# Kernel tuning notes

Measured on AMD Instinct MI355X. Metric: run time of the kernel, lower is better.

The kernel has to match this reference:

```python
import jax, jax.numpy as jnp
import numpy as np

N, E, D_IN, D_OUT = 100000, 3200000, 128, 128


def setup_inputs() -> dict:
    key = jax.random.key(0)
    ks = jax.random.split(key, 6)
    return {
        "x": jax.random.normal(ks[0], (N, D_IN), dtype=jnp.float32),
        "row": jax.random.randint(ks[1], (E,), 0, N),
        "col": jax.random.randint(ks[2], (E,), 0, N),
        "W0": jax.random.normal(ks[3], (D_OUT, D_IN), dtype=jnp.float32) * (1.0 / np.sqrt(D_IN)),
        "b0": jnp.zeros((D_OUT,), jnp.float32),
        "W1": jax.random.normal(ks[4], (D_OUT, D_IN), dtype=jnp.float32) * (1.0 / np.sqrt(D_IN)),
        "b1": jnp.zeros((D_OUT,), jnp.float32),
        "att": jax.random.normal(ks[5], (2 * D_OUT,), dtype=jnp.float32) * 0.1,
        "scale0": jnp.ones((D_OUT,), jnp.float32),
        "offset0": jnp.zeros((D_OUT,), jnp.float32),
        "scale1": jnp.ones((D_OUT,), jnp.float32),
        "offset1": jnp.zeros((D_OUT,), jnp.float32),
    }


def _norm(f, scale, offset):
    # per-node normalization over feature dim (bias='norm' branch)
    m = jnp.mean(f, axis=1, keepdims=True)
    v = jnp.var(f, axis=1, keepdims=True) + 1e-9
    return (f - m) * scale * jax.lax.rsqrt(v) + offset


def reference(x, row, col, W0, b0, W1, b1, att, scale0, offset0, scale1, offset1):
    d = W0.shape[0]
    # order-0 (self) and order-1 (neighbor) feature transforms, act='relu'
    h0 = jax.nn.relu(x @ W0.T + b0)  # [N, d]
    h1 = jax.nn.relu(x @ W1.T + b1)  # [N, d]
    # unnormalized GAT attention (no softmax), LeakyReLU(0.2)
    a_self = jax.nn.leaky_relu(h0 @ att[:d], negative_slope=0.2)   # [N]
    a_neigh = jax.nn.leaky_relu(h1 @ att[d:], negative_slope=0.2)  # [N]
    e = a_self[row] + a_neigh[col]                                 # [E]
    # SpMM: out[i] = sum_{(i,j) in edges} e_ij * h1[j]
    agg = jax.ops.segment_sum(e[:, None] * h1[col], row, num_segments=h0.shape[0])
    # batch-norm style normalization per head, then mean-aggregate over orders
    out = _norm(h0, scale0, offset0) + _norm(agg, scale1, offset1)
    return out
```

## Files before the change

### kernel.cpp

```cpp
#include <hip/hip_runtime.h>
#include <hip/hip_bf16.h>

constexpr int D = 128;
constexpr int BUCKET_SHIFT = 6;
constexpr int BUCKET_CAP_LOG2 = 12;
constexpr int BUCKET_CAP = 1 << BUCKET_CAP_LOG2;
constexpr int SEG_SHIFT = 13;
constexpr int NSEG = 13;
constexpr int BINS_PER_BUCKET = 4 * NSEG * 16;
constexpr int BINS_PER_WAVE = NSEG * 16;
constexpr int ROWSTRIDE = 130;
typedef __hip_bfloat16 bf16;

__global__ __launch_bounds__(256) void k_gemm(
    const float* __restrict__ x,
    const float* __restrict__ W0, const float* __restrict__ b0,
    const float* __restrict__ W1, const float* __restrict__ b1,
    const float* __restrict__ att,
    float* __restrict__ h0, bf16* __restrict__ h1b,
    float* __restrict__ a_self, float* __restrict__ a_neigh, int N)
{
  constexpr int XS_STRIDE = 132;
  constexpr int WS_STRIDE = 68;
  __shared__ float xs_t[64 * XS_STRIDE];
  __shared__ float ws_t[64 * WS_STRIDE];

  const int t  = threadIdx.x;
  const int nb = blockIdx.x;
  const int fb = blockIdx.y;
  const int n0 = nb * 128;

  const float* __restrict__ W    = (fb < 2) ? W0 : W1;
  const float* __restrict__ bias = (fb < 2) ? b0 : b1;
  float* __restrict__ adest      = (fb < 2) ? a_self : a_neigh;
  const int frow0 = (fb & 1) * 64;

  const int tf = t & 15;
  const int tn = t >> 4;

  const int x_nq = t >> 1;
  const int x_kq = t & 1;
  const int w_f  = t >> 2;
  const int w_kq = t & 3;

  float acc[8][4];
#pragma unroll
  for (int i = 0; i < 8; ++i)
#pragma unroll
    for (int j = 0; j < 4; ++j) acc[i][j] = 0.0f;

  const bool x_ok = (n0 + x_nq) < N;
  const float* xrow = x + (size_t)(n0 + x_nq) * D;
  const float* wrow = W + (size_t)(frow0 + w_f) * D;

  for (int c = 0; c < 2; ++c) {
    const int k0 = c * 64;
    if (c) __syncthreads();

#pragma unroll
    for (int i = 0; i < 8; ++i) {
      const int k = x_kq * 32 + i * 4;
      float4 v = x_ok ? *reinterpret_cast<const float4*>(xrow + k0 + k)
                      : make_float4(0.f, 0.f, 0.f, 0.f);
      xs_t[(k + 0) * XS_STRIDE + x_nq] = v.x;
      xs_t[(k + 1) * XS_STRIDE + x_nq] = v.y;
      xs_t[(k + 2) * XS_STRIDE + x_nq] = v.z;
      xs_t[(k + 3) * XS_STRIDE + x_nq] = v.w;
    }
#pragma unroll
    for (int i = 0; i < 4; ++i) {
      const int k = w_kq * 4 + i * 16;
      float4 v = *reinterpret_cast<const float4*>(wrow + k0 + k);
      ws_t[(k + 0) * WS_STRIDE + w_f] = v.x;
      ws_t[(k + 1) * WS_STRIDE + w_f] = v.y;
      ws_t[(k + 2) * WS_STRIDE + w_f] = v.z;
      ws_t[(k + 3) * WS_STRIDE + w_f] = v.w;
    }
    __syncthreads();

#pragma unroll 4
    for (int k = 0; k < 64; ++k) {
      const float4 a0 = *reinterpret_cast<const float4*>(&xs_t[k * XS_STRIDE + tn * 4]);
      const float4 a1 = *reinterpret_cast<const float4*>(&xs_t[k * XS_STRIDE + 64 + tn * 4]);
      const float4 bvec = *reinterpret_cast<const float4*>(&ws_t[k * WS_STRIDE + tf * 4]);
      const float av[8] = {a0.x, a0.y, a0.z, a0.w, a1.x, a1.y, a1.z, a1.w};
      const float bv[4] = {bvec.x, bvec.y, bvec.z, bvec.w};
#pragma unroll
      for (int i = 0; i < 8; ++i)
#pragma unroll
        for (int j = 0; j < 4; ++j)
          acc[i][j] = fmaf(av[i], bv[j], acc[i][j]);
    }
  }

  const float4 b4 = *reinterpret_cast<const float4*>(&bias[frow0 + tf * 4]);
  const float4 at4 = *reinterpret_cast<const float4*>(
      &att[(fb < 2 ? 0 : 128) + frow0 + tf * 4]);
#pragma unroll
  for (int i = 0; i < 8; ++i) {
    const int nq = (i < 4) ? (tn * 4 + i) : (64 + tn * 4 + (i - 4));
    const int node = n0 + nq;
    float4 r;
    r.x = fmaxf(acc[i][0] + b4.x, 0.0f);
    r.y = fmaxf(acc[i][1] + b4.y, 0.0f);
    r.z = fmaxf(acc[i][2] + b4.z, 0.0f);
    r.w = fmaxf(acc[i][3] + b4.w, 0.0f);
    float pdot = r.x * at4.x + r.y * at4.y + r.z * at4.z + r.w * at4.w;
#pragma unroll
    for (int m2 = 1; m2 < 16; m2 <<= 1) pdot += __shfl_xor(pdot, m2, 16);
    if (node < N) {
      if (fb < 2) {
        *reinterpret_cast<float4*>(&h0[(size_t)node * D + frow0 + tf * 4]) = r;
      } else {
        bf16 p[4] = {__float2bfloat16(r.x), __float2bfloat16(r.y),
                     __float2bfloat16(r.z), __float2bfloat16(r.w)};
        *reinterpret_cast<ushort4*>(&h1b[(size_t)node * D + frow0 + tf * 4]) =
            *reinterpret_cast<const ushort4*>(p);
      }
      if (tf == 0) atomicAdd(&adest[node], pdot);
    }
  }
}

__global__ __launch_bounds__(512) void k_binA(
    const int* __restrict__ row, const int* __restrict__ col,
    int* __restrict__ bukCnt, unsigned* __restrict__ buf1, int E, int NBUK)
{
  constexpr int EPB = 16384;
  __shared__ int hist[1600];
  __shared__ int base[1600];
  const int t = threadIdx.x;
  const int e0 = blockIdx.x * EPB;
  const int e1 = min(e0 + EPB, E);

  for (int i = t; i < NBUK; i += 512) hist[i] = 0;
  __syncthreads();
  for (int e = e0 + t; e < e1; e += 512)
    atomicAdd(&hist[row[e] >> BUCKET_SHIFT], 1);
  __syncthreads();
  for (int bk = t; bk < NBUK; bk += 512) {
    int c = hist[bk];
    base[bk] = (c > 0) ? atomicAdd(&bukCnt[bk], c) : 0;
  }
  __syncthreads();
  for (int i = t; i < NBUK; i += 512) hist[i] = 0;
  __syncthreads();
  for (int e = e0 + t; e < e1; e += 512) {
    int r = row[e];
    int c = col[e];
    int bk = r >> BUCKET_SHIFT;
    int pos = base[bk] + atomicAdd(&hist[bk], 1);
    if (pos < BUCKET_CAP)
      buf1[((size_t)bk << BUCKET_CAP_LOG2) + pos] =
          ((unsigned)c << BUCKET_SHIFT) | (unsigned)(r & 63);
  }
}

__global__ __launch_bounds__(1024) void k_scanB(
    const int* __restrict__ bukCnt, int* __restrict__ bukBase,
    int* __restrict__ runs, int NBUK)
{
  __shared__ int sd[1024];
  __shared__ int carry;
  const int t = threadIdx.x;
  if (t == 0) carry = 0;
  __syncthreads();
  for (int r = 0; r * 1024 < NBUK; ++r) {
    const int idx = r * 1024 + t;
    const int v = (idx < NBUK) ? min(bukCnt[idx], BUCKET_CAP) : 0;
    sd[t] = v;
    __syncthreads();
    for (int d2 = 1; d2 < 1024; d2 <<= 1) {
      int o = (t >= d2) ? sd[t - d2] : 0;
      __syncthreads();
      sd[t] += o;
      __syncthreads();
    }
    const int c0 = carry;
    if (idx < NBUK) bukBase[idx] = c0 + sd[t] - v;
    __syncthreads();
    if (t == 1023) carry = c0 + sd[1023];
    __syncthreads();
  }
  if (t == 0) runs[(size_t)NBUK * BINS_PER_BUCKET] = carry;
}

__global__ __launch_bounds__(256) void k_fine(
    const unsigned* __restrict__ buf1,
    const int* __restrict__ bukCnt, const int* __restrict__ bukBase,
    const float* __restrict__ a_self, const float* __restrict__ a_neigh,
    int* __restrict__ runs, int2* __restrict__ colS2, int N)
{
  __shared__ int lhist[BINS_PER_BUCKET], labs[BINS_PER_BUCKET], lcur[BINS_PER_BUCKET];
  __shared__ float asF[64];
  __shared__ int sd[256];
  const int b = blockIdx.x;
  const int t = threadIdx.x;
  const int n = min(bukCnt[b], BUCKET_CAP);
  const unsigned* src = buf1 + ((size_t)b << BUCKET_CAP_LOG2);
  const int rstart = b << BUCKET_SHIFT;

  for (int i = t; i < BINS_PER_BUCKET; i += 256) { lhist[i] = 0; lcur[i] = 0; }
  if (t < 64) {
    float v = (rstart + t < N) ? a_self[rstart + t] : 0.f;
    asF[t] = v > 0.f ? v : 0.2f * v;
  }
  __syncthreads();
  for (int i = t; i < n; i += 256) {
    unsigned e = src[i];
    int r = e & 63, c = e >> BUCKET_SHIFT;
    int bin = (((r >> 4) * NSEG) + (c >> SEG_SHIFT)) * 16 + (r & 15);
    atomicAdd(&lhist[bin], 1);
  }
  __syncthreads();
  int v[4], s = 0;
  const int bin0 = t * 4;
#pragma unroll
  for (int i = 0; i < 4; ++i) {
    v[i] = (bin0 + i < BINS_PER_BUCKET) ? lhist[bin0 + i] : 0;
    s += v[i];
  }
  sd[t] = s;
  __syncthreads();
  for (int d2 = 1; d2 < 256; d2 <<= 1) {
    int o = (t >= d2) ? sd[t - d2] : 0;
    __syncthreads();
    sd[t] += o;
    __syncthreads();
  }
  int excl = sd[t] - s;
  const int gb = bukBase[b];
#pragma unroll
  for (int i = 0; i < 4; ++i) {
    if (bin0 + i < BINS_PER_BUCKET) {
      labs[bin0 + i] = gb + excl;
      runs[(size_t)b * BINS_PER_BUCKET + bin0 + i] = gb + excl;
    }
    excl += v[i];
  }
  __syncthreads();
  for (int i = t; i < n; i += 256) {
    unsigned e = src[i];
    int r = e & 63, c = e >> BUCKET_SHIFT;
    int bin = (((r >> 4) * NSEG) + (c >> SEG_SHIFT)) * 16 + (r & 15);
    int pos = labs[bin] + atomicAdd(&lcur[bin], 1);
    float an = a_neigh[c];
    an = an > 0.f ? an : 0.2f * an;
    colS2[pos] = make_int2((c << 8) | r, __float_as_int(asF[r] + an));
  }
}

__global__ __launch_bounds__(256) void k_agg(
    const float* __restrict__ h0, const bf16* __restrict__ h1b,
    const int* __restrict__ runs, const int2* __restrict__ colS2,
    const float* __restrict__ scale0, const float* __restrict__ offset0,
    const float* __restrict__ scale1, const float* __restrict__ offset1,
    float* __restrict__ out, int N)
{
  __shared__ float aggL[64 * ROWSTRIDE];
  __shared__ int wb[5];
  __shared__ int2 je[4][64];
  const int b = blockIdx.x;
  const int t = threadIdx.x;
  const int w = t >> 6, l = t & 63;
  const int rbase = b << 6;

  for (int i = t; i < 64 * ROWSTRIDE; i += 256) aggL[i] = 0.f;
  if (t < 5) wb[t] = runs[(size_t)b * BINS_PER_BUCKET + (size_t)t * BINS_PER_WAVE];
  __syncthreads();

  const char* h1c = reinterpret_cast<const char*>(h1b) + l * 4;
  int2* jw = je[w];
  float acc0 = 0.f, acc1 = 0.f;
  int curRow = -1;

  auto flush = [&]() {
    float* pp = &aggL[curRow * ROWSTRIDE + 2 * l];
    const float2 o = *reinterpret_cast<const float2*>(pp);
    *reinterpret_cast<float2*>(pp) = make_float2(o.x + acc0, o.y + acc1);
  };
  auto proc = [&](int2 q, unsigned u) {
    const int r_ = q.x & 63;
    if (r_ != curRow) {
      if (curRow >= 0) flush();
      acc0 = 0.f; acc1 = 0.f; curRow = r_;
    }
    const float wg = __int_as_float(q.y);
    acc0 = fmaf(wg, __uint_as_float(u << 16), acc0);
    acc1 = fmaf(wg, __uint_as_float(u & 0xffff0000u), acc1);
  };
  auto ld = [&](int2 q) -> unsigned {
    return *reinterpret_cast<const unsigned*>(
        h1c + (size_t)((unsigned)q.x & 0xFFFFFF00u));
  };

  const int wbeg = wb[w];
  const int wend = wb[w + 1];

  if (wbeg < wend) {
    const int last = wend - 1;
    int2 P = colS2[min(wbeg + l, last)];

    int cur = wbeg;
    while (cur < wend) {
      const int m = min(64, wend - cur);
      if (l < m) jw[l] = P;
      const int2 Pn = colS2[min(cur + 64 + l, last)];

      int k = 0;
      for (; k + 16 <= m; k += 16) {
        int2 q[16]; unsigned u[16];
#pragma unroll
        for (int i = 0; i < 16; ++i) q[i] = jw[k + i];
#pragma unroll
        for (int i = 0; i < 16; ++i) u[i] = ld(q[i]);
#pragma unroll
        for (int i = 0; i < 16; ++i) proc(q[i], u[i]);
      }
      for (; k + 4 <= m; k += 4) {
        const int2 q0 = jw[k], q1 = jw[k + 1], q2 = jw[k + 2], q3 = jw[k + 3];
        const unsigned u0 = ld(q0), u1 = ld(q1), u2 = ld(q2), u3 = ld(q3);
        proc(q0, u0); proc(q1, u1); proc(q2, u2); proc(q3, u3);
      }
      for (; k < m; ++k) {
        const int2 q = jw[k];
        proc(q, ld(q));
      }
      P = Pn;
      cur += m;
    }
    if (curRow >= 0) flush();
  }
  __syncthreads();

  const float2 sc0 = *reinterpret_cast<const float2*>(&scale0[2 * l]);
  const float2 of0 = *reinterpret_cast<const float2*>(&offset0[2 * l]);
  const float2 sc1 = *reinterpret_cast<const float2*>(&scale1[2 * l]);
  const float2 of1 = *reinterpret_cast<const float2*>(&offset1[2 * l]);
  const float inv = 1.0f / 128.0f;
  for (int i = 0; i < 16; ++i) {
    const int node = rbase + (w << 4) + i;
    if (node >= N) break;
    const float2 hv = *reinterpret_cast<const float2*>(&h0[(size_t)node * D + 2 * l]);
    const float2 av = *reinterpret_cast<const float2*>(
        &aggL[((w << 4) + i) * ROWSTRIDE + 2 * l]);
    float sh = hv.x + hv.y, qh = hv.x * hv.x + hv.y * hv.y;
    float sa = av.x + av.y, qa = av.x * av.x + av.y * av.y;
#pragma unroll
    for (int o = 32; o; o >>= 1) {
      sh += __shfl_xor(sh, o, 64); qh += __shfl_xor(qh, o, 64);
      sa += __shfl_xor(sa, o, 64); qa += __shfl_xor(qa, o, 64);
    }
    const float m0 = sh * inv, v0 = qh * inv - m0 * m0 + 1e-9f;
    const float m1 = sa * inv, v1 = qa * inv - m1 * m1 + 1e-9f;
    const float r0 = rsqrtf(v0), r1 = rsqrtf(v1);
    float2 o2;
    o2.x = (hv.x - m0) * sc0.x * r0 + of0.x + (av.x - m1) * sc1.x * r1 + of1.x;
    o2.y = (hv.y - m0) * sc0.y * r0 + of0.y + (av.y - m1) * sc1.y * r1 + of1.y;
    *reinterpret_cast<float2*>(&out[(size_t)node * D + 2 * l]) = o2;
  }
}

extern "C" void kernel_launch(void* const* d_in, const int* in_sizes, int n_in,
                              void* d_out, int out_size, void* d_ws, size_t ws_size,
                              hipStream_t stream)
{
  const float* x       = (const float*)d_in[0];
  const int*   row     = (const int*)d_in[1];
  const int*   col     = (const int*)d_in[2];
  const float* W0      = (const float*)d_in[3];
  const float* b0      = (const float*)d_in[4];
  const float* W1      = (const float*)d_in[5];
  const float* b1      = (const float*)d_in[6];
  const float* att     = (const float*)d_in[7];
  const float* scale0  = (const float*)d_in[8];
  const float* offset0 = (const float*)d_in[9];
  const float* scale1  = (const float*)d_in[10];
  const float* offset1 = (const float*)d_in[11];

  const int N = in_sizes[0] / D;
  const int E = in_sizes[1];
  const int NBUK = (N + 63) >> BUCKET_SHIFT;

  char* ws = (char*)d_ws;
  size_t off = 0;
  auto alloc = [&](size_t bytes) -> void* {
    void* p = ws + off;
    off += (bytes + 511) & ~size_t(511);
    return p;
  };

  float*    h0      = (float*)d_out;
  bf16*     h1b     = (bf16*)alloc((size_t)N * D * sizeof(bf16));
  float*    a_self  = (float*)alloc((size_t)N * sizeof(float));
  float*    a_neigh = (float*)alloc((size_t)N * sizeof(float));
  int*      bukCnt  = (int*)alloc((size_t)NBUK * sizeof(int));
  int*      bukBase = (int*)alloc((size_t)NBUK * sizeof(int));
  int*      runsT   = (int*)alloc(((size_t)NBUK * BINS_PER_BUCKET + 1) * sizeof(int));
  unsigned* buf1    = (unsigned*)alloc(((size_t)NBUK << BUCKET_CAP_LOG2) * sizeof(unsigned));
  int2*     colS2   = (int2*)alloc((size_t)E * sizeof(int2));

  hipMemsetAsync(a_self, 0, (size_t)N * sizeof(float), stream);
  hipMemsetAsync(a_neigh, 0, (size_t)N * sizeof(float), stream);
  hipMemsetAsync(bukCnt, 0, (size_t)NBUK * sizeof(int), stream);

  dim3 ggrid((N + 127) / 128, 4);
  k_gemm<<<ggrid, 256, 0, stream>>>(x, W0, b0, W1, b1, att, h0, h1b,
                                    a_self, a_neigh, N);
  const int NBLKA = (E + 16383) / 16384;
  k_binA<<<NBLKA, 512, 0, stream>>>(row, col, bukCnt, buf1, E, NBUK);
  k_scanB<<<1, 1024, 0, stream>>>(bukCnt, bukBase, runsT, NBUK);
  k_fine<<<NBUK, 256, 0, stream>>>(buf1, bukCnt, bukBase, a_self, a_neigh,
                                   runsT, colS2, N);
  k_agg<<<NBUK, 256, 0, stream>>>(h0, h1b, runsT, colS2,
                                  scale0, offset0, scale1, offset1,
                                  (float*)d_out, N);
}
```

Baseline: 333.9 us.

## Fuse fine binning and aggregation into one kernel using LDS edge buffer

Merges k_fine and k_agg into a single per-bucket kernel that sorts the bucket's edges into shared memory, then aggregates them directly, and removes the global scan kernel since offsets become bucket-local. This drops the global colS2 write and read round-trip (~E*8 bytes each way) and two launches. In exchange, LDS use grows to about 32KB for aggL, 32KB for edgesL and the histograms, which lowers occupancy. It also drops the ROWSTRIDE padding, so aggL accesses may hit more bank conflicts.

```diff
diff --git a/kernel.cpp b/kernel.cpp
--- a/kernel.cpp
+++ b/kernel.cpp
@@ -9,7 +9,6 @@
 constexpr int NSEG = 13;
 constexpr int BINS_PER_BUCKET = 4 * NSEG * 16;
 constexpr int BINS_PER_WAVE = NSEG * 16;
-constexpr int ROWSTRIDE = 130;
 typedef __hip_bfloat16 bf16;
 
 __global__ __launch_bounds__(256) void k_gemm(
@@ -156,56 +155,36 @@
   }
 }
 
-__global__ __launch_bounds__(1024) void k_scanB(
-    const int* __restrict__ bukCnt, int* __restrict__ bukBase,
-    int* __restrict__ runs, int NBUK)
+__global__ __launch_bounds__(256) void k_fuse(
+    const float* __restrict__ h0, const bf16* __restrict__ h1b,
+    const unsigned* __restrict__ buf1, const int* __restrict__ bukCnt,
+    const float* __restrict__ a_self, const float* __restrict__ a_neigh,
+    const float* __restrict__ scale0, const float* __restrict__ offset0,
+    const float* __restrict__ scale1, const float* __restrict__ offset1,
+    float* __restrict__ out, int N)
 {
-  __shared__ int sd[1024];
-  __shared__ int carry;
-  const int t = threadIdx.x;
-  if (t == 0) carry = 0;
-  __syncthreads();
-  for (int r = 0; r * 1024 < NBUK; ++r) {
-    const int idx = r * 1024 + t;
-    const int v = (idx < NBUK) ? min(bukCnt[idx], BUCKET_CAP) : 0;
-    sd[t] = v;
-    __syncthreads();
-    for (int d2 = 1; d2 < 1024; d2 <<= 1) {
-      int o = (t >= d2) ? sd[t - d2] : 0;
-      __syncthreads();
-      sd[t] += o;
-      __syncthreads();
-    }
-    const int c0 = carry;
-    if (idx < NBUK) bukBase[idx] = c0 + sd[t] - v;
-    __syncthreads();
-    if (t == 1023) carry = c0 + sd[1023];
-    __syncthreads();
-  }
-  if (t == 0) runs[(size_t)NBUK * BINS_PER_BUCKET] = carry;
-}
-
-__global__ __launch_bounds__(256) void k_fine(
-    const unsigned* __restrict__ buf1,
-    const int* __restrict__ bukCnt, const int* __restrict__ bukBase,
-    const float* __restrict__ a_self, const float* __restrict__ a_neigh,
-    int* __restrict__ runs, int2* __restrict__ colS2, int N)
-{
-  __shared__ int lhist[BINS_PER_BUCKET], labs[BINS_PER_BUCKET], lcur[BINS_PER_BUCKET];
+  __shared__ float aggL[64 * 128];
+  __shared__ int2  edgesL[BUCKET_CAP];
+  __shared__ int   lhist[BINS_PER_BUCKET];
+  __shared__ int   lcur[BINS_PER_BUCKET];
+  __shared__ int   sd[256];
   __shared__ float asF[64];
-  __shared__ int sd[256];
   const int b = blockIdx.x;
   const int t = threadIdx.x;
+  const int w = t >> 6, l = t & 63;
+  const int rbase = b << 6;
+
   const int n = min(bukCnt[b], BUCKET_CAP);
   const unsigned* src = buf1 + ((size_t)b << BUCKET_CAP_LOG2);
-  const int rstart = b << BUCKET_SHIFT;
-
+
+  for (int i = t; i < 64 * 128; i += 256) aggL[i] = 0.f;
   for (int i = t; i < BINS_PER_BUCKET; i += 256) { lhist[i] = 0; lcur[i] = 0; }
   if (t < 64) {
-    float v = (rstart + t < N) ? a_self[rstart + t] : 0.f;
+    float v = (rbase + t < N) ? a_self[rbase + t] : 0.f;
     asF[t] = v > 0.f ? v : 0.2f * v;
   }
   __syncthreads();
+
   for (int i = t; i < n; i += 256) {
     unsigned e = src[i];
     int r = e & 63, c = e >> BUCKET_SHIFT;
@@ -213,12 +192,12 @@
     atomicAdd(&lhist[bin], 1);
   }
   __syncthreads();
-  int v[4], s = 0;
+  int v4[4], s = 0;
   const int bin0 = t * 4;
 #pragma unroll
   for (int i = 0; i < 4; ++i) {
-    v[i] = (bin0 + i < BINS_PER_BUCKET) ? lhist[bin0 + i] : 0;
-    s += v[i];
+    v4[i] = (bin0 + i < BINS_PER_BUCKET) ? lhist[bin0 + i] : 0;
+    s += v4[i];
   }
   sd[t] = s;
   __syncthreads();
@@ -229,53 +208,30 @@
     __syncthreads();
   }
   int excl = sd[t] - s;
-  const int gb = bukBase[b];
 #pragma unroll
   for (int i = 0; i < 4; ++i) {
-    if (bin0 + i < BINS_PER_BUCKET) {
-      labs[bin0 + i] = gb + excl;
-      runs[(size_t)b * BINS_PER_BUCKET + bin0 + i] = gb + excl;
-    }
-    excl += v[i];
+    if (bin0 + i < BINS_PER_BUCKET) lhist[bin0 + i] = excl;
+    excl += v4[i];
   }
   __syncthreads();
   for (int i = t; i < n; i += 256) {
     unsigned e = src[i];
     int r = e & 63, c = e >> BUCKET_SHIFT;
     int bin = (((r >> 4) * NSEG) + (c >> SEG_SHIFT)) * 16 + (r & 15);
-    int pos = labs[bin] + atomicAdd(&lcur[bin], 1);
+    int pos = lhist[bin] + atomicAdd(&lcur[bin], 1);
     float an = a_neigh[c];
     an = an > 0.f ? an : 0.2f * an;
-    colS2[pos] = make_int2((c << 8) | r, __float_as_int(asF[r] + an));
-  }
-}
-
-__global__ __launch_bounds__(256) void k_agg(
-    const float* __restrict__ h0, const bf16* __restrict__ h1b,
-    const int* __restrict__ runs, const int2* __restrict__ colS2,
-    const float* __restrict__ scale0, const float* __restrict__ offset0,
-    const float* __restrict__ scale1, const float* __restrict__ offset1,
-    float* __restrict__ out, int N)
-{
-  __shared__ float aggL[64 * ROWSTRIDE];
-  __shared__ int wb[5];
-  __shared__ int2 je[4][64];
-  const int b = blockIdx.x;
-  const int t = threadIdx.x;
-  const int w = t >> 6, l = t & 63;
-  const int rbase = b << 6;
-
-  for (int i = t; i < 64 * ROWSTRIDE; i += 256) aggL[i] = 0.f;
-  if (t < 5) wb[t] = runs[(size_t)b * BINS_PER_BUCKET + (size_t)t * BINS_PER_WAVE];
-  __syncthreads();
-
-  const char* h1c = reinterpret_cast<const char*>(h1b) + l * 4;
-  int2* jw = je[w];
+    edgesL[pos] = make_int2((int)(((unsigned)c << 8) | (unsigned)r),
+                            __float_as_int(asF[r] + an));
+  }
+  __syncthreads();
+
+  const char* __restrict__ h1c = reinterpret_cast<const char*>(h1b) + l * 4;
   float acc0 = 0.f, acc1 = 0.f;
   int curRow = -1;
 
   auto flush = [&]() {
-    float* pp = &aggL[curRow * ROWSTRIDE + 2 * l];
+    float* pp = &aggL[(curRow << 7) + 2 * l];
     const float2 o = *reinterpret_cast<const float2*>(pp);
     *reinterpret_cast<float2*>(pp) = make_float2(o.x + acc0, o.y + acc1);
   };
@@ -294,43 +250,29 @@
         h1c + (size_t)((unsigned)q.x & 0xFFFFFF00u));
   };
 
-  const int wbeg = wb[w];
-  const int wend = wb[w + 1];
-
-  if (wbeg < wend) {
-    const int last = wend - 1;
-    int2 P = colS2[min(wbeg + l, last)];
-
-    int cur = wbeg;
-    while (cur < wend) {
-      const int m = min(64, wend - cur);
-      if (l < m) jw[l] = P;
-      const int2 Pn = colS2[min(cur + 64 + l, last)];
-
-      int k = 0;
-      for (; k + 16 <= m; k += 16) {
-        int2 q[16]; unsigned u[16];
-#pragma unroll
-        for (int i = 0; i < 16; ++i) q[i] = jw[k + i];
-#pragma unroll
-        for (int i = 0; i < 16; ++i) u[i] = ld(q[i]);
-#pragma unroll
-        for (int i = 0; i < 16; ++i) proc(q[i], u[i]);
-      }
-      for (; k + 4 <= m; k += 4) {
-        const int2 q0 = jw[k], q1 = jw[k + 1], q2 = jw[k + 2], q3 = jw[k + 3];
-        const unsigned u0 = ld(q0), u1 = ld(q1), u2 = ld(q2), u3 = ld(q3);
-        proc(q0, u0); proc(q1, u1); proc(q2, u2); proc(q3, u3);
-      }
-      for (; k < m; ++k) {
-        const int2 q = jw[k];
-        proc(q, ld(q));
-      }
-      P = Pn;
-      cur += m;
-    }
-    if (curRow >= 0) flush();
-  }
+  const int wbeg = lhist[w * BINS_PER_WAVE];
+  const int wend = (w < 3) ? lhist[(w + 1) * BINS_PER_WAVE] : n;
+
+  int k = wbeg;
+  for (; k + 16 <= wend; k += 16) {
+    int2 q[16]; unsigned u[16];
+#pragma unroll
+    for (int i = 0; i < 16; ++i) q[i] = edgesL[k + i];
+#pragma unroll
+    for (int i = 0; i < 16; ++i) u[i] = ld(q[i]);
+#pragma unroll
+    for (int i = 0; i < 16; ++i) proc(q[i], u[i]);
+  }
+  for (; k + 4 <= wend; k += 4) {
+    const int2 q0 = edgesL[k], q1 = edgesL[k + 1], q2 = edgesL[k + 2], q3 = edgesL[k + 3];
+    const unsigned u0 = ld(q0), u1 = ld(q1), u2 = ld(q2), u3 = ld(q3);
+    proc(q0, u0); proc(q1, u1); proc(q2, u2); proc(q3, u3);
+  }
+  for (; k < wend; ++k) {
+    const int2 q = edgesL[k];
+    proc(q, ld(q));
+  }
+  if (curRow >= 0) flush();
   __syncthreads();
 
   const float2 sc0 = *reinterpret_cast<const float2*>(&scale0[2 * l]);
@@ -339,11 +281,11 @@
   const float2 of1 = *reinterpret_cast<const float2*>(&offset1[2 * l]);
   const float inv = 1.0f / 128.0f;
   for (int i = 0; i < 16; ++i) {
-    const int node = rbase + (w << 4) + i;
+    const int rl = (w << 4) + i;
+    const int node = rbase + rl;
     if (node >= N) break;
     const float2 hv = *reinterpret_cast<const float2*>(&h0[(size_t)node * D + 2 * l]);
-    const float2 av = *reinterpret_cast<const float2*>(
-        &aggL[((w << 4) + i) * ROWSTRIDE + 2 * l]);
+    const float2 av = *reinterpret_cast<const float2*>(&aggL[(rl << 7) + 2 * l]);
     float sh = hv.x + hv.y, qh = hv.x * hv.x + hv.y * hv.y;
     float sa = av.x + av.y, qa = av.x * av.x + av.y * av.y;
 #pragma unroll
@@ -395,10 +337,7 @@
   float*    a_self  = (float*)alloc((size_t)N * sizeof(float));
   float*    a_neigh = (float*)alloc((size_t)N * sizeof(float));
   int*      bukCnt  = (int*)alloc((size_t)NBUK * sizeof(int));
-  int*      bukBase = (int*)alloc((size_t)NBUK * sizeof(int));
-  int*      runsT   = (int*)alloc(((size_t)NBUK * BINS_PER_BUCKET + 1) * sizeof(int));
   unsigned* buf1    = (unsigned*)alloc(((size_t)NBUK << BUCKET_CAP_LOG2) * sizeof(unsigned));
-  int2*     colS2   = (int2*)alloc((size_t)E * sizeof(int2));
 
   hipMemsetAsync(a_self, 0, (size_t)N * sizeof(float), stream);
   hipMemsetAsync(a_neigh, 0, (size_t)N * sizeof(float), stream);
@@ -409,10 +348,7 @@
                                     a_self, a_neigh, N);
   const int NBLKA = (E + 16383) / 16384;
   k_binA<<<NBLKA, 512, 0, stream>>>(row, col, bukCnt, buf1, E, NBUK);
-  k_scanB<<<1, 1024, 0, stream>>>(bukCnt, bukBase, runsT, NBUK);
-  k_fine<<<NBUK, 256, 0, stream>>>(buf1, bukCnt, bukBase, a_self, a_neigh,
-                                   runsT, colS2, N);
-  k_agg<<<NBUK, 256, 0, stream>>>(h0, h1b, runsT, colS2,
-                                  scale0, offset0, scale1, offset1,
-                                  (float*)d_out, N);
+  k_fuse<<<NBUK, 256, 0, stream>>>(h0, h1b, buf1, bukCnt, a_self, a_neigh,
+                                   scale0, offset0, scale1, offset1,
+                                   (float*)d_out, N);
 }
```

After: 389.6 us. +16.7%, slower.

## Switch node feature GEMM to bf16 MFMA with pre-converted weights

Applied to the files above, without the earlier changes.

Replaces the FP32 shared-memory tiled GEMM with a bf16 MFMA 16x16x32 kernel. Each wave computes 16 nodes by all 128 output features, and a new small kernel converts W0/W1 to bf16 first. Because each block now covers the full feature dimension, the attention dot products are written directly, which removes the atomics and the two memsets. The cost is bf16 rounding of x and W in the GEMM, which also affects h0 and the attention scores, plus scalar (non-vectorized) stores of h0/h1.

```diff
diff --git a/kernel.cpp b/kernel.cpp
--- a/kernel.cpp
+++ b/kernel.cpp
@@ -11,113 +11,101 @@
 constexpr int BINS_PER_WAVE = NSEG * 16;
 constexpr int ROWSTRIDE = 130;
 typedef __hip_bfloat16 bf16;
+typedef __attribute__((ext_vector_type(8))) short bf16x8;
+typedef __attribute__((ext_vector_type(4))) float f32x4;
+
+__device__ __forceinline__ short f2b(float f) {
+  bf16 h = __float2bfloat16(f);
+  return *reinterpret_cast<short*>(&h);
+}
+
+__global__ void k_cvtW(const float* __restrict__ W0, const float* __restrict__ W1,
+                       short* __restrict__ Wb0, short* __restrict__ Wb1)
+{
+  int i = blockIdx.x * 256 + threadIdx.x;
+  if (i < 16384) Wb0[i] = f2b(W0[i]);
+  else if (i < 32768) { int j = i - 16384; Wb1[j] = f2b(W1[j]); }
+}
 
 __global__ __launch_bounds__(256) void k_gemm(
     const float* __restrict__ x,
-    const float* __restrict__ W0, const float* __restrict__ b0,
-    const float* __restrict__ W1, const float* __restrict__ b1,
+    const short* __restrict__ Wb0, const float* __restrict__ b0,
+    const short* __restrict__ Wb1, const float* __restrict__ b1,
     const float* __restrict__ att,
     float* __restrict__ h0, bf16* __restrict__ h1b,
     float* __restrict__ a_self, float* __restrict__ a_neigh, int N)
 {
-  constexpr int XS_STRIDE = 132;
-  constexpr int WS_STRIDE = 68;
-  __shared__ float xs_t[64 * XS_STRIDE];
-  __shared__ float ws_t[64 * WS_STRIDE];
-
-  const int t  = threadIdx.x;
-  const int nb = blockIdx.x;
+  const int t = threadIdx.x;
+  const int wv = t >> 6;
+  const int l = t & 63;
   const int fb = blockIdx.y;
-  const int n0 = nb * 128;
-
-  const float* __restrict__ W    = (fb < 2) ? W0 : W1;
-  const float* __restrict__ bias = (fb < 2) ? b0 : b1;
-  float* __restrict__ adest      = (fb < 2) ? a_self : a_neigh;
-  const int frow0 = (fb & 1) * 64;
-
-  const int tf = t & 15;
-  const int tn = t >> 4;
-
-  const int x_nq = t >> 1;
-  const int x_kq = t & 1;
-  const int w_f  = t >> 2;
-  const int w_kq = t & 3;
-
-  float acc[8][4];
-#pragma unroll
-  for (int i = 0; i < 8; ++i)
-#pragma unroll
-    for (int j = 0; j < 4; ++j) acc[i][j] = 0.0f;
-
-  const bool x_ok = (n0 + x_nq) < N;
-  const float* xrow = x + (size_t)(n0 + x_nq) * D;
-  const float* wrow = W + (size_t)(frow0 + w_f) * D;
-
-  for (int c = 0; c < 2; ++c) {
-    const int k0 = c * 64;
-    if (c) __syncthreads();
-
-#pragma unroll
-    for (int i = 0; i < 8; ++i) {
-      const int k = x_kq * 32 + i * 4;
-      float4 v = x_ok ? *reinterpret_cast<const float4*>(xrow + k0 + k)
-                      : make_float4(0.f, 0.f, 0.f, 0.f);
-      xs_t[(k + 0) * XS_STRIDE + x_nq] = v.x;
-      xs_t[(k + 1) * XS_STRIDE + x_nq] = v.y;
-      xs_t[(k + 2) * XS_STRIDE + x_nq] = v.z;
-      xs_t[(k + 3) * XS_STRIDE + x_nq] = v.w;
-    }
-#pragma unroll
-    for (int i = 0; i < 4; ++i) {
-      const int k = w_kq * 4 + i * 16;
-      float4 v = *reinterpret_cast<const float4*>(wrow + k0 + k);
-      ws_t[(k + 0) * WS_STRIDE + w_f] = v.x;
-      ws_t[(k + 1) * WS_STRIDE + w_f] = v.y;
-      ws_t[(k + 2) * WS_STRIDE + w_f] = v.z;
-      ws_t[(k + 3) * WS_STRIDE + w_f] = v.w;
-    }
-    __syncthreads();
-
-#pragma unroll 4
-    for (int k = 0; k < 64; ++k) {
-      const float4 a0 = *reinterpret_cast<const float4*>(&xs_t[k * XS_STRIDE + tn * 4]);
-      const float4 a1 = *reinterpret_cast<const float4*>(&xs_t[k * XS_STRIDE + 64 + tn * 4]);
-      const float4 bvec = *reinterpret_cast<const float4*>(&ws_t[k * WS_STRIDE + tf * 4]);
-      const float av[8] = {a0.x, a0.y, a0.z, a0.w, a1.x, a1.y, a1.z, a1.w};
-      const float bv[4] = {bvec.x, bvec.y, bvec.z, bvec.w};
-#pragma unroll
-      for (int i = 0; i < 8; ++i)
-#pragma unroll
-        for (int j = 0; j < 4; ++j)
-          acc[i][j] = fmaf(av[i], bv[j], acc[i][j]);
-    }
-  }
-
-  const float4 b4 = *reinterpret_cast<const float4*>(&bias[frow0 + tf * 4]);
-  const float4 at4 = *reinterpret_cast<const float4*>(
-      &att[(fb < 2 ? 0 : 128) + frow0 + tf * 4]);
-#pragma unroll
-  for (int i = 0; i < 8; ++i) {
-    const int nq = (i < 4) ? (tn * 4 + i) : (64 + tn * 4 + (i - 4));
-    const int node = n0 + nq;
-    float4 r;
-    r.x = fmaxf(acc[i][0] + b4.x, 0.0f);
-    r.y = fmaxf(acc[i][1] + b4.y, 0.0f);
-    r.z = fmaxf(acc[i][2] + b4.z, 0.0f);
-    r.w = fmaxf(acc[i][3] + b4.w, 0.0f);
-    float pdot = r.x * at4.x + r.y * at4.y + r.z * at4.z + r.w * at4.w;
-#pragma unroll
-    for (int m2 = 1; m2 < 16; m2 <<= 1) pdot += __shfl_xor(pdot, m2, 16);
-    if (node < N) {
-      if (fb < 2) {
-        *reinterpret_cast<float4*>(&h0[(size_t)node * D + frow0 + tf * 4]) = r;
-      } else {
-        bf16 p[4] = {__float2bfloat16(r.x), __float2bfloat16(r.y),
-                     __float2bfloat16(r.z), __float2bfloat16(r.w)};
-        *reinterpret_cast<ushort4*>(&h1b[(size_t)node * D + frow0 + tf * 4]) =
-            *reinterpret_cast<const ushort4*>(p);
+  const int nbase = blockIdx.x * 64 + wv * 16;
+  const int lm = l & 15;
+  const int lk = l >> 4;
+
+  const short* __restrict__ W    = fb ? Wb1 : Wb0;
+  const float* __restrict__ bias = fb ? b1 : b0;
+  const float* __restrict__ attp = att + fb * 128;
+
+  f32x4 acc[8];
+#pragma unroll
+  for (int i = 0; i < 8; ++i) acc[i] = (f32x4){0.f, 0.f, 0.f, 0.f};
+
+  const int node_a = nbase + lm;
+  const bool okA = node_a < N;
+  const float* xrow = x + (size_t)node_a * D + lk * 8;
+
+#pragma unroll
+  for (int ks = 0; ks < 4; ++ks) {
+    float4 a0, a1;
+    if (okA) {
+      a0 = *reinterpret_cast<const float4*>(xrow + ks * 32);
+      a1 = *reinterpret_cast<const float4*>(xrow + ks * 32 + 4);
+    } else {
+      a0 = make_float4(0.f, 0.f, 0.f, 0.f);
+      a1 = a0;
+    }
+    bf16x8 af;
+    af[0] = f2b(a0.x); af[1] = f2b(a0.y); af[2] = f2b(a0.z); af[3] = f2b(a0.w);
+    af[4] = f2b(a1.x); af[5] = f2b(a1.y); af[6] = f2b(a1.z); af[7] = f2b(a1.w);
+#pragma unroll
+    for (int nt = 0; nt < 8; ++nt) {
+      const bf16x8 bfr = *reinterpret_cast<const bf16x8*>(
+          W + (size_t)(nt * 16 + lm) * D + ks * 32 + lk * 8);
+      acc[nt] = __builtin_amdgcn_mfma_f32_16x16x32_bf16(af, bfr, acc[nt], 0, 0, 0);
+    }
+  }
+
+  float pd[4] = {0.f, 0.f, 0.f, 0.f};
+#pragma unroll
+  for (int nt = 0; nt < 8; ++nt) {
+    const int f = nt * 16 + lm;
+    const float bv = bias[f];
+    const float av = attp[f];
+#pragma unroll
+    for (int j = 0; j < 4; ++j) {
+      const float r = fmaxf(acc[nt][j] + bv, 0.f);
+      pd[j] = fmaf(r, av, pd[j]);
+      const int ng = nbase + lk * 4 + j;
+      if (ng < N) {
+        if (fb == 0) h0[(size_t)ng * D + f] = r;
+        else         h1b[(size_t)ng * D + f] = __float2bfloat16(r);
       }
-      if (tf == 0) atomicAdd(&adest[node], pdot);
+    }
+  }
+#pragma unroll
+  for (int m2 = 1; m2 < 16; m2 <<= 1) {
+    pd[0] += __shfl_xor(pd[0], m2, 16);
+    pd[1] += __shfl_xor(pd[1], m2, 16);
+    pd[2] += __shfl_xor(pd[2], m2, 16);
+    pd[3] += __shfl_xor(pd[3], m2, 16);
+  }
+  if (lm == 0) {
+    float* __restrict__ adest = fb ? a_neigh : a_self;
+#pragma unroll
+    for (int j = 0; j < 4; ++j) {
+      const int ng = nbase + lk * 4 + j;
+      if (ng < N) adest[ng] = pd[j];
     }
   }
 }
@@ -394,18 +382,19 @@
   bf16*     h1b     = (bf16*)alloc((size_t)N * D * sizeof(bf16));
   float*    a_self  = (float*)alloc((size_t)N * sizeof(float));
   float*    a_neigh = (float*)alloc((size_t)N * sizeof(float));
+  short*    Wb0     = (short*)alloc(16384 * sizeof(short));
+  short*    Wb1     = (short*)alloc(16384 * sizeof(short));
   int*      bukCnt  = (int*)alloc((size_t)NBUK * sizeof(int));
   int*      bukBase = (int*)alloc((size_t)NBUK * sizeof(int));
   int*      runsT   = (int*)alloc(((size_t)NBUK * BINS_PER_BUCKET + 1) * sizeof(int));
   unsigned* buf1    = (unsigned*)alloc(((size_t)NBUK << BUCKET_CAP_LOG2) * sizeof(unsigned));
   int2*     colS2   = (int2*)alloc((size_t)E * sizeof(int2));
 
-  hipMemsetAsync(a_self, 0, (size_t)N * sizeof(float), stream);
-  hipMemsetAsync(a_neigh, 0, (size_t)N * sizeof(float), stream);
   hipMemsetAsync(bukCnt, 0, (size_t)NBUK * sizeof(int), stream);
 
-  dim3 ggrid((N + 127) / 128, 4);
-  k_gemm<<<ggrid, 256, 0, stream>>>(x, W0, b0, W1, b1, att, h0, h1b,
+  k_cvtW<<<128, 256, 0, stream>>>(W0, W1, Wb0, Wb1);
+  dim3 ggrid((N + 63) / 64, 2);
+  k_gemm<<<ggrid, 256, 0, stream>>>(x, Wb0, b0, Wb1, b1, att, h0, h1b,
                                     a_self, a_neigh, N);
   const int NBLKA = (E + 16383) / 16384;
   k_binA<<<NBLKA, 512, 0, stream>>>(row, col, bukCnt, buf1, E, NBUK);
```

Result: faster. 292.1 us (-12.5%).
